# Kernel optimization log

Measured on AMD Instinct MI355X. Metric: run time of the kernel, lower is better.

The kernel has to match this reference:

```python
import jax, jax.numpy as jnp
import numpy as np
from jax import lax

LN_EPS = 1e-5

def _conv1d(h, w, b):
    # h: [N, L, Cin], w: [Cout, Cin, K] (torch Conv1d layout), padding=1
    out = lax.conv_general_dilated(h, w, window_strides=(1,), padding=[(1, 1)],
                                   dimension_numbers=("NWC", "OIW", "NWC"))
    return out + b

def _layer_norm(h, g, b):
    m = jnp.mean(h, axis=-1, keepdims=True)
    v = jnp.mean((h - m) ** 2, axis=-1, keepdims=True)
    return (h - m) * lax.rsqrt(v + LN_EPS) * g + b

def setup_inputs() -> dict:
    key = jax.random.key(0)
    ks = jax.random.split(key, 8)
    N, L, D, F = 32, 512, 384, 256
    return {
        "x": jax.random.normal(ks[0], (N, L, D), jnp.float32),
        "conv1_w": jax.random.normal(ks[1], (F, D, 3), jnp.float32) * 0.05,
        "conv1_b": jnp.zeros((F,), jnp.float32),
        "ln1_g": jnp.ones((F,), jnp.float32),
        "ln1_b": jnp.zeros((F,), jnp.float32),
        "conv2_w": jax.random.normal(ks[2], (F, F, 3), jnp.float32) * 0.05,
        "conv2_b": jnp.zeros((F,), jnp.float32),
        "ln2_g": jnp.ones((F,), jnp.float32),
        "ln2_b": jnp.zeros((F,), jnp.float32),
        "lin_w": jax.random.normal(ks[3], (F,), jnp.float32) * 0.05,
        "lin_b": jnp.zeros((), jnp.float32),
        "target": jax.random.randint(ks[4], (N, L), 0, 8, dtype=jnp.int32),
        "mel_max_length": 2048,
    }

def reference(x, conv1_w, conv1_b, ln1_g, ln1_b, conv2_w, conv2_b, ln2_g, ln2_b,
              lin_w, lin_b, target, mel_max_length):
    # Duration predictor (dropout is identity at inference)
    h = jax.nn.relu(_layer_norm(_conv1d(x, conv1_w, conv1_b), ln1_g, ln1_b))
    h = jax.nn.relu(_layer_norm(_conv1d(h, conv2_w, conv2_b), ln2_g, ln2_b))
    duration_predictor_output = jnp.einsum("nlf,f->nl", h, lin_w) + lin_b  # [N, L]

    # LR: frame t copies phoneme j iff cumsum(dur)[:j] <= t < cumsum(dur)[:j+1]
    # (equivalent to the one-hot alignment matmul, padded to mel_max_length)
    N, L, D = x.shape
    T = mel_max_length
    cums = jnp.cumsum(target, axis=-1)                      # [N, L]
    frames = jnp.arange(T, dtype=cums.dtype)                # [T]
    idx = jax.vmap(lambda c: jnp.searchsorted(c, frames, side="right"))(cums)  # [N, T]
    valid = frames[None, :] < cums[:, -1:]                  # frames beyond total are zero
    gathered = jnp.take_along_axis(x, jnp.clip(idx, 0, L - 1)[:, :, None], axis=1)
    output = gathered * valid[:, :, None].astype(x.dtype)   # [N, T, D]
    return output, duration_predictor_output
```

## Files before the change

kernel.cpp:

```cpp
#include <hip/hip_runtime.h>
#include <hip/hip_bf16.h>

typedef unsigned short u16;
typedef short s8v __attribute__((ext_vector_type(8)));
typedef float f4v __attribute__((ext_vector_type(4)));
typedef u16 u16x8 __attribute__((ext_vector_type(8)));

static __device__ __forceinline__ u16 f2bf(float v) {
    __hip_bfloat16 h = __float2bfloat16(v);
    return *(u16*)&h;
}

__global__ __launch_bounds__(256) void gather_prep_kernel(
    const float* __restrict__ x,
    const int*   __restrict__ target,
    const float* __restrict__ w1,
    const float* __restrict__ w2,
    u16* __restrict__ Wt1,
    u16* __restrict__ Wt2,
    float* __restrict__ out0)
{
    __shared__ int c[512];
    __shared__ int ridx[64];
    const int b = blockIdx.x, tid = threadIdx.x;

    if (b >= 1024) {
        if (b < 2176) {
            const int K = 1152, DIN = 384;
            int e = (b - 1024) * 256 + tid;
            int f = e / K;
            int rem = e - f * K;
            int kc = rem / DIN;
            int d = rem - kc * DIN;
            Wt1[e] = f2bf(w1[f * K + d * 3 + kc]);
        } else {
            const int K = 768, DIN = 256;
            int e = (b - 2176) * 256 + tid;
            int f = e / K;
            int rem = e - f * K;
            int kc = rem / DIN;
            int d = rem - kc * DIN;
            Wt2[e] = f2bf(w2[f * K + d * 3 + kc]);
        }
        return;
    }

    const int n = b >> 5, sub = b & 31;
    c[tid]       = target[n * 512 + tid];
    c[tid + 256] = target[n * 512 + 256 + tid];
    __syncthreads();
    for (int off = 1; off < 512; off <<= 1) {
        int v0 = (tid       >= off) ? c[tid       - off] : 0;
        int v1 = (tid + 256 >= off) ? c[tid + 256 - off] : 0;
        __syncthreads();
        c[tid]       += v0;
        c[tid + 256] += v1;
        __syncthreads();
    }
    const int total = c[511];
    if (tid < 64) {
        int t = sub * 64 + tid;
        int lo = 0, hi = 512;
        while (lo < hi) {
            int mid = (lo + hi) >> 1;
            if (c[mid] <= t) lo = mid + 1; else hi = mid;
        }
        ridx[tid] = (t < total) ? min(lo, 511) : -1;
    }
    __syncthreads();

    const size_t xbase = (size_t)(n << 9) * 384;
    const size_t obase = ((size_t)(n << 11) + sub * 64) * 384;
    #pragma unroll 4
    for (int it = 0; it < 12; ++it) {
        int u  = tid + it * 256;
        int j  = u % 48;
        int rl = u / 48;
        int ie = ridx[rl];
        f4v v0 = {0.f, 0.f, 0.f, 0.f}, v1 = v0;
        if (ie >= 0) {
            const float* src = &x[xbase + (size_t)ie * 384];
            v0 = *(const f4v*)&src[j * 4];
            v1 = *(const f4v*)&src[(j + 48) * 4];
        }
        float* dst = &out0[obase + (size_t)rl * 384];
        __builtin_nontemporal_store(v0, (f4v*)&dst[j * 4]);
        __builtin_nontemporal_store(v1, (f4v*)&dst[(j + 48) * 4]);
    }
}

__global__ __launch_bounds__(256, 2) void fused_conv_kernel(
    const float* __restrict__ x,
    const u16* __restrict__ Wt1,
    const u16* __restrict__ Wt2,
    const float* __restrict__ cb1, const float* __restrict__ g1,
    const float* __restrict__ bb1,
    const float* __restrict__ cb2, const float* __restrict__ g2,
    const float* __restrict__ bb2,
    const float* __restrict__ lw, const float* __restrict__ lbp,
    float* __restrict__ dpo)
{
    __shared__ __align__(128) char LDS[73216];
    char* Bs0   = LDS + 38400;
    float* redS = (float*)(LDS + 71168);
    float* redQ = (float*)(LDS + 71936);
    float* redP = (float*)(LDS + 72704);

    const int tid  = threadIdx.x;
    const int lane = tid & 63, wc = tid >> 6;
    const int lr = lane & 15, q4 = lane >> 4;
    const int sb = (blockIdx.x & 7) * 64 + (blockIdx.x >> 3);
    const int m0 = sb * 32;
    const int n  = m0 >> 9, l0 = m0 & 511;

    const int b_r32   = tid >> 2;
    const int b_slot32 = (tid & 3) ^ ((tid >> 3) & 3);
    int boff[4];
    #pragma unroll
    for (int ni = 0; ni < 4; ni++) boff[ni] = (64 * wc + 16 * ni + lr) * 64;
    const int bslot = (q4 ^ ((lr >> 1) & 3)) << 4;

    for (int u = tid; u < 2400; u += 256) {
        int j = u / 48, s = u - j * 48;
        int lp = l0 - 9 + j;
        f4v v0 = {0.f, 0.f, 0.f, 0.f}, v1 = v0;
        if (lp >= 0 && lp < 512) {
            const float* src = x + ((size_t)((n << 9) + lp)) * 384 + s * 8;
            v0 = *(const f4v*)src;
            v1 = *(const f4v*)(src + 4);
        }
        u16x8 r;
        #pragma unroll
        for (int jj = 0; jj < 4; jj++) { r[jj] = f2bf(v0[jj]); r[4 + jj] = f2bf(v1[jj]); }
        int ss = (s & ~7) | ((s & 7) ^ (j & 7));
        *(u16x8*)(LDS + j * 768 + ss * 16) = r;
    }

    auto xwread = [&](int j, int s) -> s8v {
        int ss = (s & ~7) | ((s & 7) ^ (j & 7));
        return *(const s8v*)(LDS + j * 768 + (ss << 4));
    };

    auto stageB = [&](const u16* __restrict__ Wt, int K, int buf, int t) {
        const int k0 = t * 32;
        const u16* bsrc = Wt + (size_t)b_r32 * K + k0 + b_slot32 * 8;
        char* Bs = Bs0 + buf * 16384;
        #pragma unroll
        for (int q = 0; q < 4; q++) {
            __builtin_amdgcn_global_load_lds(
                (const __attribute__((address_space(1))) void*)(bsrc + (size_t)q * 64 * K),
                (__attribute__((address_space(3))) void*)(Bs + q * 4096 + tid * 16),
                16, 0, 0);
        }
    };

    f4v acc[3][4];
    #pragma unroll
    for (int mi = 0; mi < 3; mi++)
        #pragma unroll
        for (int ni = 0; ni < 4; ni++) acc[mi][ni] = {0.f, 0.f, 0.f, 0.f};

    stageB(Wt1, 1152, 0, 0);
    __syncthreads();
    int cur = 0;
    for (int t = 0; t < 36; ++t) {
        if (t + 1 < 36) stageB(Wt1, 1152, cur ^ 1, t + 1);
        {
            char* Bs = Bs0 + cur * 16384;
            const int kc = t / 12;
            const int s  = (t % 12) * 4 + q4;
            s8v a0 = xwread(lr + kc,      s);
            s8v a1 = xwread(16 + lr + kc, s);
            s8v a2 = xwread(32 + lr + kc, s);
            s8v b0 = *(const s8v*)(Bs + boff[0] + bslot);
            s8v b1 = *(const s8v*)(Bs + boff[1] + bslot);
            s8v b2 = *(const s8v*)(Bs + boff[2] + bslot);
            s8v b3 = *(const s8v*)(Bs + boff[3] + bslot);
            acc[0][0] = __builtin_amdgcn_mfma_f32_16x16x32_bf16(a0, b0, acc[0][0], 0, 0, 0);
            acc[0][1] = __builtin_amdgcn_mfma_f32_16x16x32_bf16(a0, b1, acc[0][1], 0, 0, 0);
            acc[0][2] = __builtin_amdgcn_mfma_f32_16x16x32_bf16(a0, b2, acc[0][2], 0, 0, 0);
            acc[0][3] = __builtin_amdgcn_mfma_f32_16x16x32_bf16(a0, b3, acc[0][3], 0, 0, 0);
            acc[1][0] = __builtin_amdgcn_mfma_f32_16x16x32_bf16(a1, b0, acc[1][0], 0, 0, 0);
            acc[1][1] = __builtin_amdgcn_mfma_f32_16x16x32_bf16(a1, b1, acc[1][1], 0, 0, 0);
            acc[1][2] = __builtin_amdgcn_mfma_f32_16x16x32_bf16(a1, b2, acc[1][2], 0, 0, 0);
            acc[1][3] = __builtin_amdgcn_mfma_f32_16x16x32_bf16(a1, b3, acc[1][3], 0, 0, 0);
            acc[2][0] = __builtin_amdgcn_mfma_f32_16x16x32_bf16(a2, b0, acc[2][0], 0, 0, 0);
            acc[2][1] = __builtin_amdgcn_mfma_f32_16x16x32_bf16(a2, b1, acc[2][1], 0, 0, 0);
            acc[2][2] = __builtin_amdgcn_mfma_f32_16x16x32_bf16(a2, b2, acc[2][2], 0, 0, 0);
            acc[2][3] = __builtin_amdgcn_mfma_f32_16x16x32_bf16(a2, b3, acc[2][3], 0, 0, 0);
        }
        __syncthreads();
        cur ^= 1;
    }

    int col[4];
    float cbv[4], gv[4], bbv[4];
    #pragma unroll
    for (int ni = 0; ni < 4; ni++) {
        col[ni] = 64 * wc + 16 * ni + lr;
        cbv[ni] = cb1[col[ni]]; gv[ni] = g1[col[ni]]; bbv[ni] = bb1[col[ni]];
    }

    #pragma unroll
    for (int mi = 0; mi < 3; mi++)
        #pragma unroll
        for (int reg = 0; reg < 4; reg++) {
            float s = 0.f, q = 0.f;
            #pragma unroll
            for (int ni = 0; ni < 4; ni++) {
                float v = acc[mi][ni][reg] + cbv[ni];
                s += v; q += v * v;
            }
            #pragma unroll
            for (int msk = 1; msk < 16; msk <<= 1) {
                s += __shfl_xor(s, msk);
                q += __shfl_xor(q, msk);
            }
            if (lr == 0) {
                int rl = 16 * mi + 4 * q4 + reg;
                redS[rl * 4 + wc] = s;
                redQ[rl * 4 + wc] = q;
            }
        }
    __syncthreads();

    #pragma unroll
    for (int mi = 0; mi < 3; mi++)
        #pragma unroll
        for (int reg = 0; reg < 4; reg++) {
            int rl = 16 * mi + 4 * q4 + reg;
            int h  = rl - 7;
            if (h >= 0 && h < 34) {
                float4 ps = *(float4*)&redS[rl * 4];
                float4 pq = *(float4*)&redQ[rl * 4];
                float mean = (ps.x + ps.y + ps.z + ps.w) * (1.f / 256.f);
                float var  = (pq.x + pq.y + pq.z + pq.w) * (1.f / 256.f) - mean * mean;
                float rs   = rsqrtf(var + 1e-5f);
                int l = l0 - 8 + rl;
                bool lv = (l >= 0 && l < 512);
                #pragma unroll
                for (int ni = 0; ni < 4; ni++) {
                    float v = acc[mi][ni][reg] + cbv[ni];
                    float o = lv ? fmaxf(0.f, (v - mean) * rs * gv[ni] + bbv[ni]) : 0.f;
                    int slot = (col[ni] >> 3) ^ (h & 7);
                    *(u16*)(LDS + h * 512 + slot * 16 + (col[ni] & 7) * 2) = f2bf(o);
                }
            }
        }

    f4v acc2[2][4];
    #pragma unroll
    for (int mi = 0; mi < 2; mi++)
        #pragma unroll
        for (int ni = 0; ni < 4; ni++) acc2[mi][ni] = {0.f, 0.f, 0.f, 0.f};

    stageB(Wt2, 768, 0, 0);
    __syncthreads();
    cur = 0;
    for (int t2 = 0; t2 < 24; ++t2) {
        if (t2 + 1 < 24) stageB(Wt2, 768, cur ^ 1, t2 + 1);
        {
            char* Bs = Bs0 + cur * 16384;
            const int kc2 = t2 >> 3;
            const int s   = (t2 & 7) * 4 + q4;
            s8v b0 = *(const s8v*)(Bs + boff[0] + bslot);
            s8v b1 = *(const s8v*)(Bs + boff[1] + bslot);
            s8v b2 = *(const s8v*)(Bs + boff[2] + bslot);
            s8v b3 = *(const s8v*)(Bs + boff[3] + bslot);
            s8v a0, a1;
            {
                int h = lr + kc2;
                a0 = *(const s8v*)(LDS + h * 512 + ((s ^ (h & 7)) << 4));
                h = 16 + lr + kc2;
                a1 = *(const s8v*)(LDS + h * 512 + ((s ^ (h & 7)) << 4));
            }
            acc2[0][0] = __builtin_amdgcn_mfma_f32_16x16x32_bf16(a0, b0, acc2[0][0], 0, 0, 0);
            acc2[0][1] = __builtin_amdgcn_mfma_f32_16x16x32_bf16(a0, b1, acc2[0][1], 0, 0, 0);
            acc2[0][2] = __builtin_amdgcn_mfma_f32_16x16x32_bf16(a0, b2, acc2[0][2], 0, 0, 0);
            acc2[0][3] = __builtin_amdgcn_mfma_f32_16x16x32_bf16(a0, b3, acc2[0][3], 0, 0, 0);
            acc2[1][0] = __builtin_amdgcn_mfma_f32_16x16x32_bf16(a1, b0, acc2[1][0], 0, 0, 0);
            acc2[1][1] = __builtin_amdgcn_mfma_f32_16x16x32_bf16(a1, b1, acc2[1][1], 0, 0, 0);
            acc2[1][2] = __builtin_amdgcn_mfma_f32_16x16x32_bf16(a1, b2, acc2[1][2], 0, 0, 0);
            acc2[1][3] = __builtin_amdgcn_mfma_f32_16x16x32_bf16(a1, b3, acc2[1][3], 0, 0, 0);
        }
        __syncthreads();
        cur ^= 1;
    }

    float cbv2[4], gv2[4], bbv2[4], lwv[4];
    #pragma unroll
    for (int ni = 0; ni < 4; ni++) {
        cbv2[ni] = cb2[col[ni]]; gv2[ni] = g2[col[ni]]; bbv2[ni] = bb2[col[ni]];
        lwv[ni]  = lw[col[ni]];
    }

    float sv[2][4], sq[2][4];
    #pragma unroll
    for (int mi = 0; mi < 2; mi++)
        #pragma unroll
        for (int reg = 0; reg < 4; reg++) {
            float s = 0.f, q = 0.f;
            #pragma unroll
            for (int ni = 0; ni < 4; ni++) {
                float v = acc2[mi][ni][reg] + cbv2[ni];
                s += v; q += v * v;
            }
            #pragma unroll
            for (int msk = 1; msk < 16; msk <<= 1) {
                s += __shfl_xor(s, msk);
                q += __shfl_xor(q, msk);
            }
            sv[mi][reg] = s; sq[mi][reg] = q;
        }
    __syncthreads();
    if (lr == 0) {
        #pragma unroll
        for (int mi = 0; mi < 2; mi++)
            #pragma unroll
            for (int reg = 0; reg < 4; reg++) {
                int rl = 16 * mi + 4 * q4 + reg;
                redS[rl * 4 + wc] = sv[mi][reg];
                redQ[rl * 4 + wc] = sq[mi][reg];
            }
    }
    __syncthreads();

    float pp[2][4];
    #pragma unroll
    for (int mi = 0; mi < 2; mi++)
        #pragma unroll
        for (int reg = 0; reg < 4; reg++) {
            int rl = 16 * mi + 4 * q4 + reg;
            float4 ps = *(float4*)&redS[rl * 4];
            float4 pq = *(float4*)&redQ[rl * 4];
            float mean = (ps.x + ps.y + ps.z + ps.w) * (1.f / 256.f);
            float var  = (pq.x + pq.y + pq.z + pq.w) * (1.f / 256.f) - mean * mean;
            float rs   = rsqrtf(var + 1e-5f);
            float p = 0.f;
            #pragma unroll
            for (int ni = 0; ni < 4; ni++) {
                float v = acc2[mi][ni][reg] + cbv2[ni];
                float o = fmaxf(0.f, (v - mean) * rs * gv2[ni] + bbv2[ni]);
                p += o * lwv[ni];
            }
            #pragma unroll
            for (int msk = 1; msk < 16; msk <<= 1) p += __shfl_xor(p, msk);
            pp[mi][reg] = p;
        }
    if (lr == 0) {
        #pragma unroll
        for (int mi = 0; mi < 2; mi++)
            #pragma unroll
            for (int reg = 0; reg < 4; reg++) {
                int rl = 16 * mi + 4 * q4 + reg;
                redP[rl * 4 + wc] = pp[mi][reg];
            }
    }
    __syncthreads();
    if (tid < 32) {
        float4 p4 = *(float4*)&redP[tid * 4];
        dpo[m0 + tid] = p4.x + p4.y + p4.z + p4.w + lbp[0];
    }
}

extern "C" void kernel_launch(void* const* d_in, const int* in_sizes, int n_in,
                              void* d_out, int out_size, void* d_ws, size_t ws_size,
                              hipStream_t stream) {
    const float* x   = (const float*)d_in[0];
    const float* w1  = (const float*)d_in[1];
    const float* b1  = (const float*)d_in[2];
    const float* g1  = (const float*)d_in[3];
    const float* bb1 = (const float*)d_in[4];
    const float* w2  = (const float*)d_in[5];
    const float* b2  = (const float*)d_in[6];
    const float* g2  = (const float*)d_in[7];
    const float* bb2 = (const float*)d_in[8];
    const float* lw  = (const float*)d_in[9];
    const float* lb  = (const float*)d_in[10];
    const int* target = (const int*)d_in[11];

    char* wsb = (char*)d_ws;
    u16*  Wt1 = (u16*)wsb;
    u16*  Wt2 = (u16*)(wsb + 589824);

    float* out0 = (float*)d_out;
    float* dpo  = out0 + (size_t)32 * 2048 * 384;

    gather_prep_kernel<<<2944, 256, 0, stream>>>(
        x, target, w1, w2, Wt1, Wt2, out0);

    fused_conv_kernel<<<512, 256, 0, stream>>>(
        x, Wt1, Wt2, b1, g1, bb1, b2, g2, bb2, lw, lb, dpo);
}
```

Baseline: 74.41 us.

## Triple-buffer weight staging with explicit vmcnt waits and shrink halo tile

Switches the B-weight LDS staging in both conv GEMM loops from double to triple buffering. Prefetches run two K-steps ahead, and explicit s_waitcnt vmcnt plus raw s_barrier replace __syncthreads, so global-to-LDS loads overlap more MFMA work. It also shrinks the x halo tile from 50 to 36 rows and clamps row indices in the read helper, freeing LDS for the third buffer. The clamp relies on rows outside the stored range never contributing to kept outputs, and the hand-written vmcnt counts must match the issued loads exactly.

```diff
diff --git a/kernel.cpp b/kernel.cpp
--- a/kernel.cpp
+++ b/kernel.cpp
@@ -100,11 +100,11 @@
     const float* __restrict__ lw, const float* __restrict__ lbp,
     float* __restrict__ dpo)
 {
-    __shared__ __align__(128) char LDS[73216];
-    char* Bs0   = LDS + 38400;
-    float* redS = (float*)(LDS + 71168);
-    float* redQ = (float*)(LDS + 71936);
-    float* redP = (float*)(LDS + 72704);
+    __shared__ __align__(128) char LDS[78848];
+    char* Bs0   = LDS + 27648;
+    float* redS = (float*)(LDS + 76800);
+    float* redQ = (float*)(LDS + 77568);
+    float* redP = (float*)(LDS + 78336);
 
     const int tid  = threadIdx.x;
     const int lane = tid & 63, wc = tid >> 6;
@@ -113,16 +113,16 @@
     const int m0 = sb * 32;
     const int n  = m0 >> 9, l0 = m0 & 511;
 
-    const int b_r32   = tid >> 2;
+    const int b_r32    = tid >> 2;
     const int b_slot32 = (tid & 3) ^ ((tid >> 3) & 3);
     int boff[4];
     #pragma unroll
     for (int ni = 0; ni < 4; ni++) boff[ni] = (64 * wc + 16 * ni + lr) * 64;
     const int bslot = (q4 ^ ((lr >> 1) & 3)) << 4;
 
-    for (int u = tid; u < 2400; u += 256) {
-        int j = u / 48, s = u - j * 48;
-        int lp = l0 - 9 + j;
+    for (int u = tid; u < 1728; u += 256) {
+        int j7 = u / 48, s = u - j7 * 48;
+        int lp = l0 - 2 + j7;
         f4v v0 = {0.f, 0.f, 0.f, 0.f}, v1 = v0;
         if (lp >= 0 && lp < 512) {
             const float* src = x + ((size_t)((n << 9) + lp)) * 384 + s * 8;
@@ -132,13 +132,14 @@
         u16x8 r;
         #pragma unroll
         for (int jj = 0; jj < 4; jj++) { r[jj] = f2bf(v0[jj]); r[4 + jj] = f2bf(v1[jj]); }
-        int ss = (s & ~7) | ((s & 7) ^ (j & 7));
-        *(u16x8*)(LDS + j * 768 + ss * 16) = r;
+        int ss = (s & ~7) | ((s & 7) ^ (j7 & 7));
+        *(u16x8*)(LDS + j7 * 768 + ss * 16) = r;
     }
 
     auto xwread = [&](int j, int s) -> s8v {
-        int ss = (s & ~7) | ((s & 7) ^ (j & 7));
-        return *(const s8v*)(LDS + j * 768 + (ss << 4));
+        int j7 = min(max(j, 7), 42) - 7;
+        int ss = (s & ~7) | ((s & 7) ^ (j7 & 7));
+        return *(const s8v*)(LDS + j7 * 768 + (ss << 4));
     };
 
     auto stageB = [&](const u16* __restrict__ Wt, int K, int buf, int t) {
@@ -161,12 +162,22 @@
         for (int ni = 0; ni < 4; ni++) acc[mi][ni] = {0.f, 0.f, 0.f, 0.f};
 
     stageB(Wt1, 1152, 0, 0);
-    __syncthreads();
-    int cur = 0;
+    stageB(Wt1, 1152, 1, 1);
+    __syncthreads();
+
     for (int t = 0; t < 36; ++t) {
-        if (t + 1 < 36) stageB(Wt1, 1152, cur ^ 1, t + 1);
+        if (t + 2 < 36) {
+            stageB(Wt1, 1152, (t + 2) % 3, t + 2);
+            asm volatile("s_waitcnt vmcnt(8)" ::: "memory");
+        } else if (t + 2 == 36) {
+            asm volatile("s_waitcnt vmcnt(4)" ::: "memory");
+        } else {
+            asm volatile("s_waitcnt vmcnt(0)" ::: "memory");
+        }
+        __builtin_amdgcn_sched_barrier(0);
+        __builtin_amdgcn_s_barrier();
         {
-            char* Bs = Bs0 + cur * 16384;
+            char* Bs = Bs0 + (t % 3) * 16384;
             const int kc = t / 12;
             const int s  = (t % 12) * 4 + q4;
             s8v a0 = xwread(lr + kc,      s);
@@ -189,8 +200,7 @@
             acc[2][2] = __builtin_amdgcn_mfma_f32_16x16x32_bf16(a2, b2, acc[2][2], 0, 0, 0);
             acc[2][3] = __builtin_amdgcn_mfma_f32_16x16x32_bf16(a2, b3, acc[2][3], 0, 0, 0);
         }
-        __syncthreads();
-        cur ^= 1;
+        __builtin_amdgcn_s_barrier();
     }
 
     int col[4];
@@ -255,12 +265,22 @@
         for (int ni = 0; ni < 4; ni++) acc2[mi][ni] = {0.f, 0.f, 0.f, 0.f};
 
     stageB(Wt2, 768, 0, 0);
-    __syncthreads();
-    cur = 0;
+    stageB(Wt2, 768, 1, 1);
+    __syncthreads();
+
     for (int t2 = 0; t2 < 24; ++t2) {
-        if (t2 + 1 < 24) stageB(Wt2, 768, cur ^ 1, t2 + 1);
+        if (t2 + 2 < 24) {
+            stageB(Wt2, 768, (t2 + 2) % 3, t2 + 2);
+            asm volatile("s_waitcnt vmcnt(8)" ::: "memory");
+        } else if (t2 + 2 == 24) {
+            asm volatile("s_waitcnt vmcnt(4)" ::: "memory");
+        } else {
+            asm volatile("s_waitcnt vmcnt(0)" ::: "memory");
+        }
+        __builtin_amdgcn_sched_barrier(0);
+        __builtin_amdgcn_s_barrier();
         {
-            char* Bs = Bs0 + cur * 16384;
+            char* Bs = Bs0 + (t2 % 3) * 16384;
             const int kc2 = t2 >> 3;
             const int s   = (t2 & 7) * 4 + q4;
             s8v b0 = *(const s8v*)(Bs + boff[0] + bslot);
@@ -283,8 +303,7 @@
             acc2[1][2] = __builtin_amdgcn_mfma_f32_16x16x32_bf16(a1, b2, acc2[1][2], 0, 0, 0);
             acc2[1][3] = __builtin_amdgcn_mfma_f32_16x16x32_bf16(a1, b3, acc2[1][3], 0, 0, 0);
         }
-        __syncthreads();
-        cur ^= 1;
+        __builtin_amdgcn_s_barrier();
     }
 
     float cbv2[4], gv2[4], bbv2[4], lwv[4];
```

After: 73.34 us. About the same (-1.4%).
